# Performance work log

Hardware: AMD Instinct MI355X
Metric: run time of the kernel (lower is better)

## Reference

```python
import jax, jax.numpy as jnp
import numpy as np

EPS_RMS = 1e-6
EPS_NORM = 1e-9


def rmsnorm(x):
    return x * jax.lax.rsqrt(jnp.mean(x * x, axis=-1, keepdims=True) + EPS_RMS)


def apply_rotary(x, cos, sin):
    # x: [b, h, s, d]; cos/sin: [1, 1, s, d//2]
    d2 = x.shape[-1] // 2
    x1, x2 = x[..., :d2], x[..., d2:]
    return jnp.concatenate([x1 * cos - x2 * sin, x1 * sin + x2 * cos], axis=-1)


def setup_inputs() -> dict:
    key = jax.random.key(0)
    ks = jax.random.split(key, 16)
    b, l, e, h = 4, 1024, 2048, 16
    d = e // h
    query = jax.random.normal(ks[0], (b, l, e), jnp.float32)
    keyt = jax.random.normal(ks[1], (b, l, e), jnp.float32)
    value = jax.random.normal(ks[2], (b, l, e), jnp.float32)
    attn_mask = jnp.tril(jnp.ones((l, l), bool))[None, None]  # causal bool mask
    cos = jax.random.normal(ks[3], (1, 1, l, d // 2), jnp.float32)
    sin = jax.random.normal(ks[4], (1, 1, l, d // 2), jnp.float32)
    sc = 0.02
    Wq = jax.random.normal(ks[5], (e, e), jnp.float32) * sc
    bq = jnp.zeros((e,), jnp.float32)
    Wk = jax.random.normal(ks[6], (e, e), jnp.float32) * sc
    bk = jnp.zeros((e,), jnp.float32)
    Wv = jax.random.normal(ks[7], (e, e), jnp.float32) * sc
    bv = jnp.zeros((e,), jnp.float32)
    Wo = jax.random.normal(ks[8], (e, e), jnp.float32) * sc
    bo = jnp.zeros((e,), jnp.float32)
    return dict(query=query, key=keyt, value=value, attn_mask=attn_mask,
                cos=cos, sin=sin, Wq=Wq, bq=bq, Wk=Wk, bk=bk,
                Wv=Wv, bv=bv, Wo=Wo, bo=bo)


def reference(query, key, value, attn_mask, cos, sin, Wq, bq, Wk, bk, Wv, bv, Wo, bo):
    b, l, e = query.shape
    s = key.shape[1]
    h = 16
    d = e // h
    q = (query @ Wq.T + bq).reshape(b, l, h, d).transpose(0, 2, 1, 3)
    k = (key @ Wk.T + bk).reshape(b, s, h, d).transpose(0, 2, 1, 3)
    v = (value @ Wv.T + bv).reshape(b, s, h, d).transpose(0, 2, 1, 3)
    q, k = rmsnorm(q), rmsnorm(k)
    # rotary (self-attention, s == l)
    q = apply_rotary(q, cos[:, :, :s], sin[:, :, :s])
    k = apply_rotary(k, cos[:, :, :s], sin[:, :, :s])
    # SDPA with boolean mask
    scores = jnp.einsum('bhld,bhsd->bhls', q, k) / jnp.sqrt(jnp.float32(d))
    scores = jnp.where(attn_mask, scores, jnp.finfo(scores.dtype).min)
    p = jax.nn.softmax(scores, axis=-1)
    o = jnp.einsum('bhls,bhsd->bhld', p, v)  # [b,h,l,d]
    # post-attention v-orthogonalization (o.shape == v.shape here)
    vnorm = jnp.sqrt(jnp.sum(v * v, axis=-1, keepdims=True))
    vn = v / jnp.maximum(vnorm, EPS_NORM)
    o = o - jnp.sum(o * vn, axis=-1, keepdims=True) * vn
    o = o.transpose(0, 2, 1, 3).reshape(b, l, e)
    return o @ Wo.T + bo
```

## Files before the change

### kernel.cpp

```cpp
#include <hip/hip_runtime.h>

typedef short short8 __attribute__((ext_vector_type(8)));
typedef float f32x4 __attribute__((ext_vector_type(4)));

#define MFMA_BF16 __builtin_amdgcn_mfma_f32_16x16x32_bf16

__device__ __forceinline__ unsigned short f2bf(float f) {
  unsigned int u = __float_as_uint(f);
  u += 0x7fffu + ((u >> 16) & 1u);
  return (unsigned short)(u >> 16);
}
__device__ __forceinline__ float bf2f(unsigned short u) {
  return __uint_as_float(((unsigned int)u) << 16);
}

typedef __attribute__((address_space(1))) const unsigned int as1_u32;
typedef __attribute__((address_space(3))) unsigned int as3_u32;
__device__ __forceinline__ void gld16(const void* g, void* l) {
  __builtin_amdgcn_global_load_lds((as1_u32*)(unsigned long long)g,
                                   (as3_u32*)(unsigned int)(unsigned long long)l,
                                   16, 0, 0);
}

template <int N>
__device__ __forceinline__ void vmwait() {
  if constexpr (N == 0) asm volatile("s_waitcnt vmcnt(0)" ::: "memory");
  else if constexpr (N == 4) asm volatile("s_waitcnt vmcnt(4)" ::: "memory");
  else if constexpr (N == 6) asm volatile("s_waitcnt vmcnt(6)" ::: "memory");
}
__device__ __forceinline__ void barrier_raw() {
  asm volatile("" ::: "memory");
  __builtin_amdgcn_s_barrier();
  asm volatile("" ::: "memory");
}

struct CvtArgs {
  const float* s[7];
  unsigned short* d[7];
  int n8[7];
};

__global__ __launch_bounds__(256) void cvtall(CvtArgs a) {
  const int seg = blockIdx.y;
  int i = blockIdx.x * 256 + threadIdx.x;
  if (i >= a.n8[seg]) return;
  const float4* s4 = (const float4*)a.s[seg];
  float4 x = s4[2 * i], y = s4[2 * i + 1];
  short8 o = {(short)f2bf(x.x), (short)f2bf(x.y), (short)f2bf(x.z), (short)f2bf(x.w),
              (short)f2bf(y.x), (short)f2bf(y.y), (short)f2bf(y.z), (short)f2bf(y.w)};
  *(short8*)&a.d[seg][(size_t)i * 8] = o;
}

struct GemmArgs {
  const unsigned short* A[3];
  const unsigned short* W[3];
  const float* bias[3];
  unsigned short* Cb[3];
  float* Cf;
};

template <bool OUTBF, int NZ, int MF>
__global__ __launch_bounds__(256, 2) void gemm_bf16(GemmArgs g) {
  extern __shared__ unsigned short Sh[];
  constexpr int NA = MF / 2;
  constexpr int L = NA + 2;
  constexpr int BOFF = MF * 1024;
  constexpr int RS = MF * 1024 + 4096;
  const int K = 2048, N = 2048, NT = 64;

  const int B = blockIdx.x;
  int z, bm, bn;
  if constexpr (MF == 8) {
    z = B >> 8;
    const int i = B & 255;
    const int xcd = i & 7, q = i >> 3;
    bm = (xcd * 2 + (q & 1)) * 256;
    bn = (q >> 1) * 128;
  } else {
    z = 0;
    const int xcd = B & 7, q = B >> 3;
    bm = (xcd * 4 + (q & 3)) * 128;
    bn = (q >> 2) * 128;
  }

  const unsigned short* __restrict__ A = g.A[z];
  const unsigned short* __restrict__ W = g.W[z];
  const float* __restrict__ bias = g.bias[z];
  unsigned short* __restrict__ Cb = g.Cb[z];

  const int t = threadIdx.x, lane = t & 63, w = t >> 6;
  const int wr = w >> 1, wc = w & 1;
  const int quad = lane >> 4, l16 = lane & 15;

  const int sk = ((lane & 3) * 8) ^ (((lane >> 3) & 3) << 3);
  const int srow = lane >> 2;
  size_t gA[NA], gB[2];
  int lA[NA], lB[2];
  for (int j = 0; j < NA; ++j) {
    gA[j] = (size_t)(bm + w * (MF * 8) + j * 16 + srow) * K + sk;
    lA[j] = (w * (MF * 8) + j * 16) * 32;
  }
  for (int j = 0; j < 2; ++j) {
    gB[j] = (size_t)(bn + w * 32 + j * 16 + srow) * K + sk;
    lB[j] = BOFF + (w * 32 + j * 16) * 32;
  }

  auto STAGE = [&](int kq, unsigned short* Ld) {
    for (int j = 0; j < NA; ++j) gld16(A + gA[j] + kq, Ld + lA[j]);
    for (int j = 0; j < 2; ++j)  gld16(W + gB[j] + kq, Ld + lB[j]);
  };

  const int ka = (quad * 8) ^ (((l16 >> 1) & 3) << 3);
  const int raA = (wr * (MF * 16) + l16) * 32 + ka;
  const int raB = BOFF + (wc * 64 + l16) * 32 + ka;

  const f32x4 fz = {0.f, 0.f, 0.f, 0.f};
  f32x4 acc[MF][4];
  for (int a = 0; a < MF; ++a)
    for (int b = 0; b < 4; ++b) acc[a][b] = fz;

  unsigned short* cur = Sh;
  unsigned short* nxt = Sh + RS;
  unsigned short* stg = Sh + 2 * RS;

  STAGE(0, cur);
  STAGE(32, nxt);
  vmwait<L>();
  barrier_raw();

  for (int tt = 0; tt < NT; ++tt) {
    short8 af[MF], bv[4];
#pragma unroll
    for (int mt = 0; mt < MF; ++mt)
      af[mt] = *(const short8*)&cur[raA + mt * 512];
#pragma unroll
    for (int nt = 0; nt < 4; ++nt)
      bv[nt] = *(const short8*)&cur[raB + nt * 512];
    if (tt + 2 < NT) STAGE((tt + 2) * 32, stg);
    __builtin_amdgcn_s_setprio(1);
#pragma unroll
    for (int mt = 0; mt < MF; ++mt)
#pragma unroll
      for (int nt = 0; nt < 4; ++nt)
        acc[mt][nt] = MFMA_BF16(af[mt], bv[nt], acc[mt][nt], 0, 0, 0);
    __builtin_amdgcn_s_setprio(0);
    if (tt < NT - 2) vmwait<L>();
    else if (tt == NT - 2) vmwait<0>();
    barrier_raw();
    unsigned short* tmp = cur; cur = nxt; nxt = stg; stg = tmp;
  }

  for (int mt = 0; mt < MF; ++mt)
    for (int nt = 0; nt < 4; ++nt) {
      int row = bm + wr * (MF * 16) + mt * 16 + quad * 4;
      int col = bn + wc * 64 + nt * 16 + l16;
      float bc = bias[col];
      for (int r2 = 0; r2 < 4; ++r2) {
        float v = acc[mt][nt][r2] + bc;
        if (OUTBF) Cb[(size_t)(row + r2) * N + col] = f2bf(v);
        else       g.Cf[(size_t)(row + r2) * N + col] = v;
      }
    }
}

__global__ __launch_bounds__(256) void rmsvt(
    const unsigned short* __restrict__ Qf, const unsigned short* __restrict__ Kf,
    const unsigned short* __restrict__ Vf,
    const float* __restrict__ cosT, const float* __restrict__ sinT,
    unsigned short* __restrict__ Qb, unsigned short* __restrict__ Kb,
    unsigned short* __restrict__ Vt) {
  __shared__ unsigned short Vsh[64 * 136];
  if (blockIdx.x < 16384) {
    const int rid = blockIdx.x * 4 + (threadIdx.x >> 6);
    const int lane = threadIdx.x & 63;
    const int li = rid & 1023;
    const int bh = rid >> 10;
    const int hi = bh & 15, bi = bh >> 4;
    const int src = (bi * 1024 + li) * 2048 + hi * 128;
    const int dst = rid * 128;
    const float c = cosT[li * 64 + lane];
    const float s = sinT[li * 64 + lane];

    float q1 = bf2f(Qf[src + lane]), q2 = bf2f(Qf[src + 64 + lane]);
    float ss = q1 * q1 + q2 * q2;
    for (int off = 32; off; off >>= 1) ss += __shfl_xor(ss, off, 64);
    float r = rsqrtf(ss * (1.f / 128.f) + 1e-6f);
    float qa = q1 * r, qb2 = q2 * r;
    const float qsc = 0.08838834764831845f * 1.4426950408889634f;
    Qb[dst + lane]      = f2bf((qa * c - qb2 * s) * qsc);
    Qb[dst + 64 + lane] = f2bf((qa * s + qb2 * c) * qsc);

    float k1 = bf2f(Kf[src + lane]), k2 = bf2f(Kf[src + 64 + lane]);
    float ks = k1 * k1 + k2 * k2;
    for (int off = 32; off; off >>= 1) ks += __shfl_xor(ks, off, 64);
    float rk = rsqrtf(ks * (1.f / 128.f) + 1e-6f);
    float ka = k1 * rk, kb2 = k2 * rk;
    Kb[dst + lane]      = f2bf(ka * c - kb2 * s);
    Kb[dst + 64 + lane] = f2bf(ka * s + kb2 * c);
  } else {
    const int bid = blockIdx.x - 16384;
    const int t = threadIdx.x;
    const int bh = bid >> 4, l0 = (bid & 15) * 64;
    const int hi = bh & 15, bi = bh >> 4;
    {
      int row = t >> 2, c4 = t & 3;
      const unsigned short* src = &Vf[(size_t)(bi * 1024 + l0 + row) * 2048 + hi * 128];
      for (int i = 0; i < 4; ++i) {
        int chunk = c4 * 4 + i;
        *(int4*)&Vsh[row * 136 + chunk * 8] = *(const int4*)&src[chunk * 8];
      }
    }
    __syncthreads();
    {
      int d = t >> 1, half = t & 1;
      unsigned short* dst = &Vt[(size_t)bh * 131072 + (size_t)d * 1024 + l0 + half * 32];
      for (int g = 0; g < 4; ++g) {
        short8 o;
        for (int j = 0; j < 8; ++j)
          o[j] = (short)Vsh[(half * 32 + g * 8 + j) * 136 + d];
        *(short8*)&dst[g * 8] = o;
      }
    }
  }
}

__global__ __launch_bounds__(512, 4) void attn(
    const unsigned short* __restrict__ Qb, const unsigned short* __restrict__ Kb,
    const unsigned short* __restrict__ Vt, unsigned short* __restrict__ Of0,
    unsigned short* __restrict__ Of1, float* __restrict__ Lb) {
  __shared__ unsigned short Kl[64 * 136];
  __shared__ unsigned short Vl[128 * 72];
  __shared__ unsigned short Pl[8][16 * 72];
  const int t = threadIdx.x, lane = t & 63, w = t >> 6;
  const int quad = lane >> 4, l16 = lane & 15;
  const int B = blockIdx.x;
  const int bh = (B & 7) + 8 * ((B >> 3) & 7);
  const int jj = B >> 6;
  const int pair = jj >> 1, split = jj & 1;
  const unsigned short* Qh = Qb + (size_t)bh * 131072;
  const unsigned short* Kh = Kb + (size_t)bh * 131072;
  const unsigned short* Vh = Vt + (size_t)bh * 131072;
  unsigned short* Oh = (split ? Of1 : Of0) + (size_t)bh * 131072;
  float* Lh = Lb + split * 65536 + bh * 1024;

  const int krow = t >> 4, kcol = (t & 15) * 8;
  const int vdr = t >> 3, vc = (t & 7) * 8;
  const f32x4 fz = {0.f, 0.f, 0.f, 0.f};

  for (int ti = 0; ti < 2; ++ti) {
    const int qt = ti == 0 ? 7 - pair : pair;
    const int q0 = qt * 128;

    short8 aQ[4];
    {
      int qr = q0 + w * 16 + l16;
      for (int kk = 0; kk < 4; ++kk)
        aQ[kk] = *(const short8*)&Qh[(size_t)qr * 128 + kk * 32 + quad * 8];
    }
    f32x4 oacc[8];
    for (int i = 0; i < 8; ++i) oacc[i] = fz;
    float Lr[4] = {0.f, 0.f, 0.f, 0.f};
    const int nST = 2 * qt + 2;

    for (int st = split; st < nST; st += 2) {
      const int s0 = st * 64;
      __syncthreads();
      {
        *(int4*)&Kl[krow * 136 + kcol] =
            *(const int4*)&Kh[(size_t)(s0 + krow) * 128 + kcol];
        *(int4*)&Kl[(krow + 32) * 136 + kcol] =
            *(const int4*)&Kh[(size_t)(s0 + krow + 32) * 128 + kcol];
        *(int4*)&Vl[vdr * 72 + vc] =
            *(const int4*)&Vh[(size_t)vdr * 1024 + s0 + vc];
        *(int4*)&Vl[(vdr + 64) * 72 + vc] =
            *(const int4*)&Vh[(size_t)(vdr + 64) * 1024 + s0 + vc];
      }
      __syncthreads();

      f32x4 sfr[4];
      for (int j = 0; j < 4; ++j) sfr[j] = fz;
      for (int kk = 0; kk < 4; ++kk)
        for (int ni = 0; ni < 4; ++ni) {
          short8 bK = *(const short8*)&Kl[(ni * 16 + l16) * 136 + kk * 32 + quad * 8];
          sfr[ni] = MFMA_BF16(aQ[kk], bK, sfr[ni], 0, 0, 0);
        }

      const bool diag = (s0 + 63 > q0);
      for (int r = 0; r < 4; ++r) {
        int q = q0 + w * 16 + quad * 4 + r;
        float ps = 0.f;
        for (int ni = 0; ni < 4; ++ni) {
          float sv = sfr[ni][r];
          if (diag && (s0 + ni * 16 + l16 > q)) sv = -30000.f;
          float pp = exp2f(sv - 16.5f);
          ps += pp;
          Pl[w][(quad * 4 + r) * 72 + ni * 16 + l16] = f2bf(pp);
        }
        ps += __shfl_xor(ps, 1, 64);
        ps += __shfl_xor(ps, 2, 64);
        ps += __shfl_xor(ps, 4, 64);
        ps += __shfl_xor(ps, 8, 64);
        Lr[r] += ps;
      }

      for (int kk = 0; kk < 2; ++kk) {
        short8 aP = *(const short8*)&Pl[w][l16 * 72 + kk * 32 + quad * 8];
        for (int nt = 0; nt < 8; ++nt) {
          short8 bV = *(const short8*)&Vl[(nt * 16 + l16) * 72 + kk * 32 + quad * 8];
          oacc[nt] = MFMA_BF16(aP, bV, oacc[nt], 0, 0, 0);
        }
      }
    }

    for (int r = 0; r < 4; ++r) {
      int q = q0 + w * 16 + quad * 4 + r;
      size_t base = (size_t)q * 128;
      for (int nt = 0; nt < 8; ++nt)
        Oh[base + nt * 16 + l16] = f2bf(oacc[nt][r]);
      if (l16 == 0) Lh[q] = Lr[r];
    }
  }
}

__global__ __launch_bounds__(256) void vnfix(
    const unsigned short* __restrict__ Of0, const unsigned short* __restrict__ Of1,
    const float* __restrict__ Lb, const unsigned short* __restrict__ Vf,
    unsigned short* __restrict__ Op) {
  const int rid = blockIdx.x * 4 + (threadIdx.x >> 6);
  const int lane = threadIdx.x & 63;
  const int li = rid & 1023;
  const int bh = rid >> 10;
  const int hi = bh & 15, bi = bh >> 4;
  const int src = (bi * 1024 + li) * 2048 + hi * 128;
  float inv = 1.f / (Lb[rid] + Lb[65536 + rid]);
  float o1 = (bf2f(Of0[(size_t)rid * 128 + lane]) + bf2f(Of1[(size_t)rid * 128 + lane])) * inv;
  float o2 = (bf2f(Of0[(size_t)rid * 128 + 64 + lane]) + bf2f(Of1[(size_t)rid * 128 + 64 + lane])) * inv;
  float v1 = bf2f(Vf[src + lane]), v2 = bf2f(Vf[src + 64 + lane]);
  float vv = v1 * v1 + v2 * v2;
  float dd = o1 * v1 + o2 * v2;
  for (int off = 32; off; off >>= 1) {
    vv += __shfl_xor(vv, off, 64);
    dd += __shfl_xor(dd, off, 64);
  }
  float vn = fmaxf(sqrtf(vv), 1e-9f);
  float tc = dd / (vn * vn);
  Op[src + lane]      = f2bf(o1 - tc * v1);
  Op[src + 64 + lane] = f2bf(o2 - tc * v2);
}

extern "C" void kernel_launch(void* const* d_in, const int* in_sizes, int n_in,
                              void* d_out, int out_size, void* d_ws, size_t ws_size,
                              hipStream_t stream) {
  const float* query = (const float*)d_in[0];
  const float* key   = (const float*)d_in[1];
  const float* value = (const float*)d_in[2];
  const float* cosT  = (const float*)d_in[4];
  const float* sinT  = (const float*)d_in[5];
  const float* Wq = (const float*)d_in[6];
  const float* bq = (const float*)d_in[7];
  const float* Wk = (const float*)d_in[8];
  const float* bk = (const float*)d_in[9];
  const float* Wv = (const float*)d_in[10];
  const float* bv = (const float*)d_in[11];
  const float* Wo = (const float*)d_in[12];
  const float* bo = (const float*)d_in[13];
  float* out = (float*)d_out;

  char* ws = (char*)d_ws;
  const size_t MB = 1048576;
  unsigned short* Xq  = (unsigned short*)(ws);
  unsigned short* Xk  = (unsigned short*)(ws + 16 * MB);
  unsigned short* Xv  = (unsigned short*)(ws + 32 * MB);
  unsigned short* Wqb = (unsigned short*)(ws + 48 * MB);
  unsigned short* Wkb = (unsigned short*)(ws + 56 * MB);
  unsigned short* Wvb = (unsigned short*)(ws + 64 * MB);
  unsigned short* Wob = (unsigned short*)(ws + 72 * MB);
  unsigned short* Qf  = (unsigned short*)(ws + 80 * MB);
  unsigned short* Kf  = (unsigned short*)(ws + 96 * MB);
  unsigned short* Vf  = (unsigned short*)(ws + 112 * MB);
  unsigned short* Qbb = Xq;
  unsigned short* Kbb = Xk;
  unsigned short* Vtb = Xv;
  unsigned short* Of0 = Qf;
  unsigned short* Of1 = Kf;
  float*          Lbp = (float*)(ws + 64 * MB);
  unsigned short* Opb = (unsigned short*)(ws + 48 * MB);

  CvtArgs ca;
  ca.s[0] = query; ca.d[0] = Xq;  ca.n8[0] = 1048576;
  ca.s[1] = key;   ca.d[1] = Xk;  ca.n8[1] = 1048576;
  ca.s[2] = value; ca.d[2] = Xv;  ca.n8[2] = 1048576;
  ca.s[3] = Wq;    ca.d[3] = Wqb; ca.n8[3] = 524288;
  ca.s[4] = Wk;    ca.d[4] = Wkb; ca.n8[4] = 524288;
  ca.s[5] = Wv;    ca.d[5] = Wvb; ca.n8[5] = 524288;
  ca.s[6] = Wo;    ca.d[6] = Wob; ca.n8[6] = 524288;
  cvtall<<<dim3(4096, 7), 256, 0, stream>>>(ca);

  GemmArgs gp;
  gp.A[0] = Xq;  gp.A[1] = Xk;  gp.A[2] = Xv;
  gp.W[0] = Wqb; gp.W[1] = Wkb; gp.W[2] = Wvb;
  gp.bias[0] = bq; gp.bias[1] = bk; gp.bias[2] = bv;
  gp.Cb[0] = Qf; gp.Cb[1] = Kf; gp.Cb[2] = Vf;
  gp.Cf = nullptr;
  gemm_bf16<true, 3, 8><<<768, 256, 73728, stream>>>(gp);

  rmsvt<<<17408, 256, 0, stream>>>(Qf, Kf, Vf, cosT, sinT, Qbb, Kbb, Vtb);

  attn<<<512, 512, 0, stream>>>(Qbb, Kbb, Vtb, Of0, Of1, Lbp);

  vnfix<<<16384, 256, 0, stream>>>(Of0, Of1, Lbp, Vf, Opb);

  GemmArgs go;
  go.A[0] = Opb; go.A[1] = nullptr; go.A[2] = nullptr;
  go.W[0] = Wob; go.W[1] = nullptr; go.W[2] = nullptr;
  go.bias[0] = bo; go.bias[1] = nullptr; go.bias[2] = nullptr;
  go.Cb[0] = nullptr; go.Cb[1] = nullptr; go.Cb[2] = nullptr;
  go.Cf = out;
  gemm_bf16<false, 1, 4><<<512, 256, 49152, stream>>>(go);
}
```

Before: 439.2 us.

## Split GEMM main loop into two half-phases interleaving A/B staging with MFMA

```diff
diff --git a/kernel.cpp b/kernel.cpp
--- a/kernel.cpp
+++ b/kernel.cpp
@@ -64,6 +64,7 @@
   extern __shared__ unsigned short Sh[];
   constexpr int NA = MF / 2;
   constexpr int L = NA + 2;
+  constexpr int MH = MF / 2;
   constexpr int BOFF = MF * 1024;
   constexpr int RS = MF * 1024 + 4096;
   const int K = 2048, N = 2048, NT = 64;
@@ -105,9 +106,11 @@
     lB[j] = BOFF + (w * 32 + j * 16) * 32;
   }
 
-  auto STAGE = [&](int kq, unsigned short* Ld) {
+  auto STAGE_A = [&](int kq, unsigned short* Ld) {
     for (int j = 0; j < NA; ++j) gld16(A + gA[j] + kq, Ld + lA[j]);
-    for (int j = 0; j < 2; ++j)  gld16(W + gB[j] + kq, Ld + lB[j]);
+  };
+  auto STAGE_B = [&](int kq, unsigned short* Ld) {
+    for (int j = 0; j < 2; ++j) gld16(W + gB[j] + kq, Ld + lB[j]);
   };
 
   const int ka = (quad * 8) ^ (((l16 >> 1) & 3) << 3);
@@ -123,30 +126,47 @@
   unsigned short* nxt = Sh + RS;
   unsigned short* stg = Sh + 2 * RS;
 
-  STAGE(0, cur);
-  STAGE(32, nxt);
+  STAGE_A(0, cur);  STAGE_B(0, cur);
+  STAGE_A(32, nxt); STAGE_B(32, nxt);
   vmwait<L>();
   barrier_raw();
 
   for (int tt = 0; tt < NT; ++tt) {
-    short8 af[MF], bv[4];
-#pragma unroll
-    for (int mt = 0; mt < MF; ++mt)
-      af[mt] = *(const short8*)&cur[raA + mt * 512];
+    short8 af0[MH], bv[4];
+#pragma unroll
+    for (int mt = 0; mt < MH; ++mt)
+      af0[mt] = *(const short8*)&cur[raA + mt * 512];
 #pragma unroll
     for (int nt = 0; nt < 4; ++nt)
       bv[nt] = *(const short8*)&cur[raB + nt * 512];
-    if (tt + 2 < NT) STAGE((tt + 2) * 32, stg);
+    if (tt + 2 < NT) STAGE_A((tt + 2) * 32, stg);
+    barrier_raw();
     __builtin_amdgcn_s_setprio(1);
 #pragma unroll
-    for (int mt = 0; mt < MF; ++mt)
+    for (int mt = 0; mt < MH; ++mt)
 #pragma unroll
       for (int nt = 0; nt < 4; ++nt)
-        acc[mt][nt] = MFMA_BF16(af[mt], bv[nt], acc[mt][nt], 0, 0, 0);
+        acc[mt][nt] = MFMA_BF16(af0[mt], bv[nt], acc[mt][nt], 0, 0, 0);
     __builtin_amdgcn_s_setprio(0);
+    barrier_raw();
+
+    short8 af1[MH];
+#pragma unroll
+    for (int mt = 0; mt < MH; ++mt)
+      af1[mt] = *(const short8*)&cur[raA + (MH + mt) * 512];
+    if (tt + 2 < NT) STAGE_B((tt + 2) * 32, stg);
     if (tt < NT - 2) vmwait<L>();
     else if (tt == NT - 2) vmwait<0>();
     barrier_raw();
+    __builtin_amdgcn_s_setprio(1);
+#pragma unroll
+    for (int mt = 0; mt < MH; ++mt)
+#pragma unroll
+      for (int nt = 0; nt < 4; ++nt)
+        acc[MH + mt][nt] = MFMA_BF16(af1[mt], bv[nt], acc[MH + mt][nt], 0, 0, 0);
+    __builtin_amdgcn_s_setprio(0);
+    barrier_raw();
+
     unsigned short* tmp = cur; cur = nxt; nxt = stg; stg = tmp;
   }
 
```

After: 436.0 us. About the same (-0.7%).
